# Kernel optimization log

Hardware: AMD Instinct MI355X
Metric: run time of the kernel (lower is better)

Reference implementation:

```python
import jax, jax.numpy as jnp
import numpy as np

NN_SIZE = 10  # matches init_kwargs nn_size


def _knn_idx(points, k):
    """points: (B,N,D). Returns (B,N,k) indices of k nearest neighbors, self excluded."""
    sq = jnp.sum(points * points, axis=-1)  # (B,N)
    # squared euclidean distances (B,N,N)
    d2 = sq[:, :, None] + sq[:, None, :] - 2.0 * jnp.einsum('bnd,bmd->bnm', points, points)
    _, idx = jax.lax.top_k(-d2, k + 1)  # smallest distances; first hit is self
    return idx[:, :, 1:]  # drop self -> (B,N,k)


def _uniform_laplacian(points, knn_idx):
    """points: (B,N,D); knn_idx: (B,N,K). lap = mean(neighbors) - point."""
    neigh = jax.vmap(lambda p, i: p[i])(points, knn_idx)  # (B,N,K,D) gather per batch
    return jnp.mean(neigh, axis=2) - points


def setup_inputs() -> dict:
    key = jax.random.key(0)
    k1, k2 = jax.random.split(key)
    B, N, D = 2, 8192, 3
    point1 = jax.random.normal(k1, (B, N, D), dtype=jnp.float32)
    point2 = jax.random.normal(k2, (B, N, D), dtype=jnp.float32)
    return {"point1": point1, "point2": point2}


def reference(point1, point2):
    knn_idx = _knn_idx(point1, NN_SIZE)          # connectivity from ref cloud
    lap1 = _uniform_laplacian(point1, knn_idx)   # (B,N,3)
    lap2 = _uniform_laplacian(point2, knn_idx)   # reuse knn_idx
    # metric = L1Loss (mean reduction); use_norm=False
    return jnp.mean(jnp.abs(lap1 - lap2))
```

## Files before the change

kernel.cpp:

```cpp
#include <hip/hip_runtime.h>
#include <math.h>


constexpr int NPTS  = 8192;
constexpr int NB    = 2;
constexpr int KNN   = 10;
constexpr int QPB   = 64;
constexpr int WPB   = 16;
constexpr int P1Q     = 32;
constexpr int P1BLOCK = P1Q * WPB;
constexpr int MVSTR   = WPB * KNN + 1;
constexpr int MASK13 = 0xFFFFE000;

constexpr int   G    = 32;
constexpr int   NC   = G * G * G;
constexpr float BMIN = -5.5f;
constexpr float BW   = 11.0f;
constexpr float H    = BW / G;
constexpr float INVH = (float)G / BW;

__device__ __forceinline__ void ins1(int l[KNN], int x) {
#pragma unroll
    for (int k = KNN - 1; k > 0; --k) l[k] = min(l[k], max(l[k - 1], x));
    l[0] = min(l[0], x);
}
__device__ __forceinline__ void ins2(int l[KNN], int a, int b) {
    const int b0 = min(a, b), b1 = max(a, b);
#pragma unroll
    for (int k = KNN - 1; k >= 2; --k)
        l[k] = min(l[k], min(max(l[k - 1], b0), max(l[k - 2], b1)));
    l[1] = min(l[1], min(max(l[0], b0), b1));
    l[0] = min(l[0], b0);
}
template<int S>
__device__ __forceinline__ void ins2s(int l[KNN], int a, int b) {
    const int b0 = min(a, b), b1 = max(a, b);
#pragma unroll
    for (int k = KNN - 1; k >= S + 2; --k)
        l[k] = min(l[k], min(max(l[k - 1], b0), max(l[k - 2], b1)));
    l[S + 1] = min(l[S + 1], min(max(l[S], b0), b1));
    l[S] = min(l[S], b0);
}
__device__ __forceinline__ void merge_sorted(int l[KNN], const int p[KNN]) {
    ins2s<0>(l, p[0], p[1]);
    ins2s<2>(l, p[2], p[3]);
    ins2s<4>(l, p[4], p[5]);
    ins2s<6>(l, p[6], p[7]);
    ins2s<8>(l, p[8], p[9]);
}

__global__ void pack_bin(const float* __restrict__ p1, float4* __restrict__ w,
                         int* __restrict__ hist, int* __restrict__ cellof,
                         float* __restrict__ out, int* __restrict__ nfail) {
    const int i = blockIdx.x * blockDim.x + threadIdx.x;
    if (i >= NB * NPTS) return;
    if (i == 0) { out[0] = 0.0f; nfail[0] = 0; }
    const float x = p1[3 * i], y = p1[3 * i + 1], z = p1[3 * i + 2];
    w[i] = make_float4(x, y, z, fmaf(x, x, fmaf(y, y, z * z)));
    const int cx = min(max((int)floorf((x - BMIN) * INVH), 0), G - 1);
    const int cy = min(max((int)floorf((y - BMIN) * INVH), 0), G - 1);
    const int cz = min(max((int)floorf((z - BMIN) * INVH), 0), G - 1);
    const int c = (cz << 10) | (cy << 5) | cx;
    cellof[i] = c;
    atomicAdd(&hist[(i >> 13) * NC + c], 1);
}

__global__ __launch_bounds__(1024)
void scan_cells(const int* __restrict__ hist, int* __restrict__ starts) {
    __shared__ int wsum[16];
    const int b = blockIdx.x, t = threadIdx.x;
    const int* hb = hist + b * NC;
    int* sb = starts + b * (NC + 1);
    const int c0 = t * 32;
    const int4* hb4 = (const int4*)(hb + c0);
    int loc[32]; int sum = 0;
#pragma unroll
    for (int j = 0; j < 8; ++j) {
        const int4 v = hb4[j];
        loc[4 * j + 0] = v.x; loc[4 * j + 1] = v.y;
        loc[4 * j + 2] = v.z; loc[4 * j + 3] = v.w;
        sum += v.x + v.y + v.z + v.w;
    }
    const int lane = t & 63, wvi = t >> 6;
    int incl = sum;
#pragma unroll
    for (int off = 1; off < 64; off <<= 1) {
        const int v = __shfl_up(incl, off);
        if (lane >= off) incl += v;
    }
    if (lane == 63) wsum[wvi] = incl;
    __syncthreads();
    if (t < 16) {
        const int v = wsum[t];
        int iv = v;
#pragma unroll
        for (int off = 1; off < 16; off <<= 1) {
            const int u = __shfl_up(iv, off);
            if (t >= off) iv += u;
        }
        wsum[t] = iv - v;
    }
    __syncthreads();
    int run = wsum[wvi] + incl - sum;
#pragma unroll
    for (int j = 0; j < 32; ++j) { sb[c0 + j] = run; run += loc[j]; }
    if (t == 1023) sb[NC] = run;
}

__global__ void scatter_all(const int* __restrict__ cellof,
                            const int* __restrict__ starts,
                            int* __restrict__ hist,
                            const float4* __restrict__ w,
                            const float* __restrict__ p2,
                            float4* __restrict__ wsorted,
                            float4* __restrict__ p2s) {
    const int i = blockIdx.x * blockDim.x + threadIdx.x;
    if (i >= NB * NPTS) return;
    const int b = i >> 13;
    const int c = cellof[i];
    const int old = atomicSub(&hist[b * NC + c], 1);
    const int pos = b * NPTS + starts[b * (NC + 1) + c] + old - 1;
    wsorted[pos] = w[i];
    p2s[pos] = make_float4(p2[3 * i], p2[3 * i + 1], p2[3 * i + 2], 0.0f);
}

template<int S>
__device__ __forceinline__ void scan_batched(const float4* __restrict__ W,
                                             const int* __restrict__ st,
                                             int cx, int cy, int cz,
                                             float m2x, float m2y, float m2z,
                                             float q2, int qpos, int sl,
                                             int l[KNN])
{
    constexpr int Wd = 2 * S + 1;
    constexpr int R  = Wd * Wd;
    constexpr int CH = 5;
    const int IMAX = 0x7FFFFFFF;
    int J0[R], J1[R];
#pragma unroll
    for (int r = 0; r < R; ++r) {
        const int dy = r % Wd - S, dz = r / Wd - S;
        const int ay = cy + dy, az = cz + dz;
        const bool ok = ((unsigned)ay < G) && ((unsigned)az < G);
        const int cbase = (az << 10) | (ay << 5);
        const int lo = cbase + max(cx - S, 0);
        const int hi = cbase + min(cx + S, G - 1) + 1;
        J0[r] = ok ? st[lo] : 0;
        J1[r] = ok ? st[hi] : 0;
    }
#pragma unroll
    for (int base = 0; base < R; base += CH) {
        float4 P[CH];
#pragma unroll
        for (int c = 0; c < CH; ++c) {
            const int r = base + c;
            if (r < R) {
                const int j = min(J0[r] + sl, NPTS - 1);
                P[c] = W[j];
            }
        }
#pragma unroll
        for (int c = 0; c < CH; ++c) {
            const int r = base + c;
            if (r < R) {
                const int j1 = J1[r];
                int j = J0[r] + sl;
                if (j < j1) {
                    float4 c4 = P[c];
                    while (true) {
                        const int jn = j + WPB;
                        const bool more = jn < j1;
                        float4 nx;
                        if (more) nx = W[jn];
                        const float d2 = fmaf(m2x, c4.x,
                                         fmaf(m2y, c4.y,
                                         fmaf(m2z, c4.z, c4.w + q2)));
                        int key = (__float_as_int(d2) & MASK13) | j;
                        key = (j == qpos) ? IMAX : key;
                        ins1(l, key);
                        if (!more) break;
                        c4 = nx; j = jn;
                    }
                }
            }
        }
    }
}

__global__ __launch_bounds__(P1BLOCK)
void phase1(const float4* __restrict__ wsorted, const float4* __restrict__ p2s,
            const int* __restrict__ starts, float* __restrict__ out,
            int* __restrict__ nfail, int* __restrict__ worklist)
{
    __shared__ int mv[P1Q * MVSTR];

    const int bid   = blockIdx.x;
    const int batch = bid & 1;
    const int g     = bid >> 1;
    const int tid   = threadIdx.x;
    const int qi    = tid >> 4;
    const int sl    = tid & 15;
    const int qpos  = (g << 5) + qi;

    const float4* W  = wsorted + batch * NPTS;
    const float4* P2 = p2s + batch * NPTS;
    const int*    st = starts + batch * (NC + 1);

    const float4 qp = W[qpos];
    const int cx = min(max((int)floorf((qp.x - BMIN) * INVH), 0), G - 1);
    const int cy = min(max((int)floorf((qp.y - BMIN) * INVH), 0), G - 1);
    const int cz = min(max((int)floorf((qp.z - BMIN) * INVH), 0), G - 1);
    const float lox = BMIN + cx * H, loy = BMIN + cy * H, loz = BMIN + cz * H;
    const float df = fminf(fminf(fminf(qp.x - lox, lox + H - qp.x),
                                 fminf(qp.y - loy, loy + H - qp.y)),
                           fminf(qp.z - loz, loz + H - qp.z));
    const float m2x = -2.0f * qp.x, m2y = -2.0f * qp.y, m2z = -2.0f * qp.z;
    const float q2 = qp.w;
    const int IMAX = 0x7FFFFFFF;

    const int sCov = (q2 > 4.8f) ? 2 : 1;

    int l[KNN];
#pragma unroll
    for (int k = 0; k < KNN; ++k) l[k] = IMAX;

    if (sCov == 1)
        scan_batched<1>(W, st, cx, cy, cz, m2x, m2y, m2z, q2, qpos, sl, l);
    else
        scan_batched<2>(W, st, cx, cy, cz, m2x, m2y, m2z, q2, qpos, sl, l);

#pragma unroll
    for (int k = 0; k < KNN; ++k) mv[qi * MVSTR + sl * KNN + k] = l[k];
    __syncthreads();

    float v = 0.0f;
    if (tid < P1Q) {
        int M[KNN];
#pragma unroll
        for (int k = 0; k < KNN; ++k) M[k] = IMAX;
#pragma unroll
        for (int e = 0; e < WPB; ++e) {
            int p[KNN];
#pragma unroll
            for (int k = 0; k < KNN; ++k) p[k] = mv[tid * MVSTR + e * KNN + k];
            merge_sorted(M, p);
        }

        const float tau = __int_as_float(M[KNN - 1] & MASK13);
        const float4 qq = W[(g << 5) + tid];
        const int sc = (qq.w > 4.8f) ? 2 : 1;
        const int qcx = min(max((int)floorf((qq.x - BMIN) * INVH), 0), G - 1);
        const int qcy = min(max((int)floorf((qq.y - BMIN) * INVH), 0), G - 1);
        const int qcz = min(max((int)floorf((qq.z - BMIN) * INVH), 0), G - 1);
        const float qlx = BMIN + qcx * H, qly = BMIN + qcy * H, qlz = BMIN + qcz * H;
        const float qdf = fminf(fminf(fminf(qq.x - qlx, qlx + H - qq.x),
                                      fminf(qq.y - qly, qly + H - qq.y)),
                                fminf(qq.z - qlz, qlz + H - qq.z));
        const float R = (float)sc * H + qdf;
        const bool covered = (tau <= R * R * 0.996f);
        if (covered) {
            float s1x = 0, s1y = 0, s1z = 0, s2x = 0, s2y = 0, s2z = 0;
#pragma unroll
            for (int k = 0; k < KNN; ++k) {
                const int j = M[k] & (NPTS - 1);
                const float4 c4 = W[j];
                const float4 n2 = P2[j];
                s1x += c4.x; s1y += c4.y; s1z += c4.z;
                s2x += n2.x; s2y += n2.y; s2z += n2.z;
            }
            const float4 p2v = P2[(g << 5) + tid];
            const float dx = (s1x * 0.1f - qq.x) - (s2x * 0.1f - p2v.x);
            const float dy2 = (s1y * 0.1f - qq.y) - (s2y * 0.1f - p2v.y);
            const float dz2 = (s1z * 0.1f - qq.z) - (s2z * 0.1f - p2v.z);
            v = fabsf(dx) + fabsf(dy2) + fabsf(dz2);
        } else {
            const int wi = atomicAdd(nfail, 1);
            worklist[wi] = (batch << 16) | ((g << 5) + tid);
        }
    }
    if (tid < 64) {
#pragma unroll
        for (int off = 32; off >= 1; off >>= 1) v += __shfl_down(v, off);
        if (tid == 0)
            atomicAdd(out, v * (1.0f / (float)(NB * NPTS * 3)));
    }
}

constexpr int P2BLK = 256;
constexpr int P2GRID = 512;

__global__ __launch_bounds__(P2BLK)
void phase2(const float4* __restrict__ wsorted, const float4* __restrict__ p2s,
            const int* __restrict__ nfail, const int* __restrict__ worklist,
            float* __restrict__ out)
{
    const int lane = threadIdx.x & 63;
    const int wv   = threadIdx.x >> 6;
    const int wid  = blockIdx.x * (P2BLK / 64) + wv;
    const int NW   = P2GRID * (P2BLK / 64);
    const int nf   = *nfail;
    const int IMAX = 0x7FFFFFFF;
    float acc = 0.0f;

    for (int i = wid; i < nf; i += NW) {
        const int e = worklist[i];
        const int batch = e >> 16, qpos = e & 0xFFFF;
        const float4* W  = wsorted + batch * NPTS;
        const float4* P2 = p2s + batch * NPTS;
        const float4 qp = W[qpos];
        const float m2x = -2.0f * qp.x, m2y = -2.0f * qp.y, m2z = -2.0f * qp.z;
        const float q2 = qp.w;

        int l[KNN];
#pragma unroll
        for (int k = 0; k < KNN; ++k) l[k] = IMAX;

#pragma unroll 2
        for (int it = 0; it < NPTS / 128; ++it) {
            const int ja = it * 128 + lane, jb = ja + 64;
            const float4 ca = W[ja];
            const float4 cb = W[jb];
            const float da = fmaf(m2x, ca.x, fmaf(m2y, ca.y, fmaf(m2z, ca.z, ca.w + q2)));
            const float db = fmaf(m2x, cb.x, fmaf(m2y, cb.y, fmaf(m2z, cb.z, cb.w + q2)));
            int ka = (__float_as_int(da) & MASK13) | ja;
            int kb = (__float_as_int(db) & MASK13) | jb;
            ka = (ja == qpos) ? IMAX : ka;
            kb = (jb == qpos) ? IMAX : kb;
            ins2(l, ka, kb);
        }
        for (int off = 1; off < 64; off <<= 1) {
            int p[KNN];
#pragma unroll
            for (int k = 0; k < KNN; ++k) p[k] = __shfl_xor(l[k], off);
            merge_sorted(l, p);
        }
        float s1x = 0, s1y = 0, s1z = 0, s2x = 0, s2y = 0, s2z = 0;
#pragma unroll
        for (int k = 0; k < KNN; ++k) {
            const int j = l[k] & (NPTS - 1);
            const float4 c4 = W[j];
            const float4 n2 = P2[j];
            s1x += c4.x; s1y += c4.y; s1z += c4.z;
            s2x += n2.x; s2y += n2.y; s2z += n2.z;
        }
        const float4 p2v = P2[qpos];
        const float dx = (s1x * 0.1f - qp.x) - (s2x * 0.1f - p2v.x);
        const float dy = (s1y * 0.1f - qp.y) - (s2y * 0.1f - p2v.y);
        const float dz = (s1z * 0.1f - qp.z) - (s2z * 0.1f - p2v.z);
        if (lane == 0) acc += fabsf(dx) + fabsf(dy) + fabsf(dz);
    }

    if (lane == 0 && acc != 0.0f)
        atomicAdd(out, acc * (1.0f / (float)(NB * NPTS * 3)));
}

constexpr int FB_WPB = 8;
constexpr int FB_BLOCK = QPB * FB_WPB;
constexpr int CHUNK = NPTS / FB_WPB;

__global__ void prep_pack(const float* __restrict__ p, float4* __restrict__ w) {
    const int i = blockIdx.x * blockDim.x + threadIdx.x;
    if (i < NB * NPTS) {
        const float x = p[3 * i], y = p[3 * i + 1], z = p[3 * i + 2];
        w[i] = make_float4(x, y, z, fmaf(x, x, fmaf(y, y, z * z)));
    }
}

__global__ __launch_bounds__(FB_BLOCK, 2)
void knn_lap(const float4* __restrict__ w1, const float* __restrict__ p2,
             float* __restrict__ out)
{
    __shared__ int mv[FB_WPB * KNN * QPB];
    const int batch = blockIdx.x >> 7;
    const int qbase = (blockIdx.x & 127) << 6;
    const int lane  = threadIdx.x & 63;
    const int wv    = __builtin_amdgcn_readfirstlane(threadIdx.x >> 6);
    const int query = qbase + lane;
    const float4* Wb = w1 + batch * NPTS;
    const float4 qp = Wb[query];
    const float m2x = -2.0f * qp.x, m2y = -2.0f * qp.y, m2z = -2.0f * qp.z;
    const float q2 = qp.w;
    const int IMAX = 0x7FFFFFFF;
    int l[KNN];
#pragma unroll
    for (int k = 0; k < KNN; ++k) l[k] = IMAX;
    const int c0 = wv * CHUNK;
    const float4* cand = Wb + c0;
#pragma unroll 4
    for (int i = 0; i < CHUNK; i += 2) {
        const float4 ca = cand[i];
        const float4 cb = cand[i + 1];
        const int ja = c0 + i, jb = ja + 1;
        const float da = fmaf(m2x, ca.x, fmaf(m2y, ca.y, fmaf(m2z, ca.z, ca.w + q2)));
        const float db = fmaf(m2x, cb.x, fmaf(m2y, cb.y, fmaf(m2z, cb.z, cb.w + q2)));
        int ka = (__float_as_int(da) & MASK13) | ja;
        int kb = (__float_as_int(db) & MASK13) | jb;
        ka = (ja == query) ? IMAX : ka;
        kb = (jb == query) ? IMAX : kb;
        ins2(l, ka, kb);
    }
#pragma unroll
    for (int k = 0; k < KNN; ++k) mv[(wv * KNN + k) * QPB + lane] = l[k];
    __syncthreads();
    if (threadIdx.x < QPB) {
        int m[KNN];
#pragma unroll
        for (int k = 0; k < KNN; ++k) m[k] = IMAX;
#pragma unroll
        for (int e = 0; e < FB_WPB; ++e) {
            int p[KNN];
#pragma unroll
            for (int k = 0; k < KNN; ++k) p[k] = mv[(e * KNN + k) * QPB + lane];
            merge_sorted(m, p);
        }
        const float* P2b = p2 + (size_t)batch * NPTS * 3;
        float s1x = 0, s1y = 0, s1z = 0, s2x = 0, s2y = 0, s2z = 0;
#pragma unroll
        for (int k = 0; k < KNN; ++k) {
            const int j = m[k] & (NPTS - 1);
            const float4 c = Wb[j];
            s1x += c.x; s1y += c.y; s1z += c.z;
            s2x += P2b[3 * j + 0]; s2y += P2b[3 * j + 1]; s2z += P2b[3 * j + 2];
        }
        const int q = qbase + threadIdx.x;
        const float p2x = P2b[3 * q + 0], p2y = P2b[3 * q + 1], p2z = P2b[3 * q + 2];
        const float dx = (s1x * 0.1f - qp.x) - (s2x * 0.1f - p2x);
        const float dy = (s1y * 0.1f - qp.y) - (s2y * 0.1f - p2y);
        const float dz = (s1z * 0.1f - qp.z) - (s2z * 0.1f - p2z);
        float v = fabsf(dx) + fabsf(dy) + fabsf(dz);
#pragma unroll
        for (int off = 32; off >= 1; off >>= 1) v += __shfl_down(v, off);
        if (threadIdx.x == 0)
            atomicAdd(out, v * (1.0f / (float)(NB * NPTS * 3)));
    }
}

extern "C" void kernel_launch(void* const* d_in, const int* in_sizes, int n_in,
                              void* d_out, int out_size, void* d_ws, size_t ws_size,
                              hipStream_t stream) {
    const float* p1 = (const float*)d_in[0];
    const float* p2 = (const float*)d_in[1];
    float* out = (float*)d_out;

    size_t off = 0;
    float4* w       = (float4*)d_ws;               off += (size_t)NB * NPTS * 16;
    int*    hist    = (int*)((char*)d_ws + off);   off += (size_t)NB * NC * 4;
    int*    starts  = (int*)((char*)d_ws + off);   off += (size_t)NB * (NC + 1) * 4 + 8;
    int*    cellof  = (int*)((char*)d_ws + off);   off += (size_t)NB * NPTS * 4;
    float4* wsorted = (float4*)((char*)d_ws + off); off += (size_t)NB * NPTS * 16;
    float4* p2s     = (float4*)((char*)d_ws + off); off += (size_t)NB * NPTS * 16;
    int*    nfail   = (int*)((char*)d_ws + off);   off += 16;
    int*    worklist= (int*)((char*)d_ws + off);   off += (size_t)NB * NPTS * 4;

    if (ws_size < off) {
        hipMemsetAsync(out, 0, sizeof(float), stream);
        prep_pack<<<(NB * NPTS + 255) / 256, 256, 0, stream>>>(p1, w);
        knn_lap<<<NB * (NPTS / QPB), FB_BLOCK, 0, stream>>>(w, p2, out);
        return;
    }

    hipMemsetAsync(hist, 0, (size_t)NB * NC * 4, stream);
    pack_bin<<<(NB * NPTS + 255) / 256, 256, 0, stream>>>(p1, w, hist, cellof,
                                                          out, nfail);
    scan_cells<<<NB, 1024, 0, stream>>>(hist, starts);
    scatter_all<<<(NB * NPTS + 255) / 256, 256, 0, stream>>>(cellof, starts, hist,
                                                             w, p2, wsorted, p2s);
    phase1<<<NB * (NPTS / P1Q), P1BLOCK, 0, stream>>>(wsorted, p2s, starts, out,
                                                      nfail, worklist);
    phase2<<<P2GRID, P2BLK, 0, stream>>>(wsorted, p2s, nfail, worklist, out);
}
```

Before: 116.5 us.

## Fuse binning, scan and scatter into one shared-memory counting-sort kernel

Replaces the memset plus three kernels (pack_bin, scan_cells, scatter_all) with a single build_all kernel that runs one 1024-thread block per batch. That block builds the cell histogram with shared-memory atomics on an XOR-swizzled index, scans it in place and scatters both point clouds. This removes three launches, the global histogram atomics and the intermediate w/cellof buffers. The cost is only two blocks of parallelism and a 128KB shared-memory footprint, so the sort runs serially on two CUs.

```diff
diff --git a/kernel.cpp b/kernel.cpp
--- a/kernel.cpp
+++ b/kernel.cpp
@@ -19,6 +19,8 @@
 constexpr float H    = BW / G;
 constexpr float INVH = (float)G / BW;
 
+__device__ __forceinline__ int SW(int c) { return c ^ ((c >> 5) & 31); }
+
 __device__ __forceinline__ void ins1(int l[KNN], int x) {
 #pragma unroll
     for (int k = KNN - 1; k > 0; --k) l[k] = min(l[k], max(l[k - 1], x));
@@ -49,79 +51,91 @@
     ins2s<8>(l, p[8], p[9]);
 }
 
-__global__ void pack_bin(const float* __restrict__ p1, float4* __restrict__ w,
-                         int* __restrict__ hist, int* __restrict__ cellof,
-                         float* __restrict__ out, int* __restrict__ nfail) {
-    const int i = blockIdx.x * blockDim.x + threadIdx.x;
-    if (i >= NB * NPTS) return;
-    if (i == 0) { out[0] = 0.0f; nfail[0] = 0; }
-    const float x = p1[3 * i], y = p1[3 * i + 1], z = p1[3 * i + 2];
-    w[i] = make_float4(x, y, z, fmaf(x, x, fmaf(y, y, z * z)));
-    const int cx = min(max((int)floorf((x - BMIN) * INVH), 0), G - 1);
-    const int cy = min(max((int)floorf((y - BMIN) * INVH), 0), G - 1);
-    const int cz = min(max((int)floorf((z - BMIN) * INVH), 0), G - 1);
-    const int c = (cz << 10) | (cy << 5) | cx;
-    cellof[i] = c;
-    atomicAdd(&hist[(i >> 13) * NC + c], 1);
-}
-
-__global__ __launch_bounds__(1024)
-void scan_cells(const int* __restrict__ hist, int* __restrict__ starts) {
-    __shared__ int wsum[16];
-    const int b = blockIdx.x, t = threadIdx.x;
-    const int* hb = hist + b * NC;
+constexpr int BB = 1024;
+constexpr int PPT = NPTS / BB;
+
+__global__ __launch_bounds__(BB)
+void build_all(const float* __restrict__ p1, const float* __restrict__ p2,
+               int* __restrict__ starts, float4* __restrict__ wsorted,
+               float4* __restrict__ p2s, float* __restrict__ out,
+               int* __restrict__ nfail)
+{
+    __shared__ unsigned int hcur[NC];
+    __shared__ int wsum[BB / 64];
+
+    const int b = blockIdx.x;
+    const int t = threadIdx.x;
+    if (b == 0 && t == 0) { out[0] = 0.0f; nfail[0] = 0; }
+
+#pragma unroll
+    for (int j = 0; j < NC / BB; ++j) hcur[t + BB * j] = 0u;
+    __syncthreads();
+
+    const float* P1 = p1 + (size_t)b * NPTS * 3;
+    float4 r[6];
+    {
+        const float4* P14 = (const float4*)P1;
+#pragma unroll
+        for (int j = 0; j < 6; ++j) r[j] = P14[t * 6 + j];
+    }
+    const float* rf = (const float*)r;
+    float px[PPT], py[PPT], pz[PPT], pw[PPT]; int pc[PPT];
+#pragma unroll
+    for (int j = 0; j < PPT; ++j) {
+        const float x = rf[3 * j], y = rf[3 * j + 1], z = rf[3 * j + 2];
+        px[j] = x; py[j] = y; pz[j] = z;
+        pw[j] = fmaf(x, x, fmaf(y, y, z * z));
+        const int cx = min(max((int)floorf((x - BMIN) * INVH), 0), G - 1);
+        const int cy = min(max((int)floorf((y - BMIN) * INVH), 0), G - 1);
+        const int cz = min(max((int)floorf((z - BMIN) * INVH), 0), G - 1);
+        pc[j] = (cz << 10) | (cy << 5) | cx;
+        atomicAdd(&hcur[SW(pc[j])], 1u);
+    }
+    __syncthreads();
+
+    const int c0 = t * 32;
+    unsigned int sum = 0;
+#pragma unroll
+    for (int j = 0; j < 32; ++j) sum += hcur[SW(c0 + j)];
+    const int lane = t & 63, wvi = t >> 6;
+    unsigned int incl = sum;
+#pragma unroll
+    for (int off = 1; off < 64; off <<= 1) {
+        const unsigned int u = __shfl_up(incl, off);
+        if (lane >= off) incl += u;
+    }
+    if (lane == 63) wsum[wvi] = (int)incl;
+    __syncthreads();
+    unsigned int woff = 0;
+    for (int e = 0; e < wvi; ++e) woff += (unsigned int)wsum[e];
+    unsigned int run = woff + incl - sum;
     int* sb = starts + b * (NC + 1);
-    const int c0 = t * 32;
-    const int4* hb4 = (const int4*)(hb + c0);
-    int loc[32]; int sum = 0;
-#pragma unroll
-    for (int j = 0; j < 8; ++j) {
-        const int4 v = hb4[j];
-        loc[4 * j + 0] = v.x; loc[4 * j + 1] = v.y;
-        loc[4 * j + 2] = v.z; loc[4 * j + 3] = v.w;
-        sum += v.x + v.y + v.z + v.w;
-    }
-    const int lane = t & 63, wvi = t >> 6;
-    int incl = sum;
-#pragma unroll
-    for (int off = 1; off < 64; off <<= 1) {
-        const int v = __shfl_up(incl, off);
-        if (lane >= off) incl += v;
-    }
-    if (lane == 63) wsum[wvi] = incl;
-    __syncthreads();
-    if (t < 16) {
-        const int v = wsum[t];
-        int iv = v;
-#pragma unroll
-        for (int off = 1; off < 16; off <<= 1) {
-            const int u = __shfl_up(iv, off);
-            if (t >= off) iv += u;
-        }
-        wsum[t] = iv - v;
-    }
-    __syncthreads();
-    int run = wsum[wvi] + incl - sum;
-#pragma unroll
-    for (int j = 0; j < 32; ++j) { sb[c0 + j] = run; run += loc[j]; }
-    if (t == 1023) sb[NC] = run;
-}
-
-__global__ void scatter_all(const int* __restrict__ cellof,
-                            const int* __restrict__ starts,
-                            int* __restrict__ hist,
-                            const float4* __restrict__ w,
-                            const float* __restrict__ p2,
-                            float4* __restrict__ wsorted,
-                            float4* __restrict__ p2s) {
-    const int i = blockIdx.x * blockDim.x + threadIdx.x;
-    if (i >= NB * NPTS) return;
-    const int b = i >> 13;
-    const int c = cellof[i];
-    const int old = atomicSub(&hist[b * NC + c], 1);
-    const int pos = b * NPTS + starts[b * (NC + 1) + c] + old - 1;
-    wsorted[pos] = w[i];
-    p2s[pos] = make_float4(p2[3 * i], p2[3 * i + 1], p2[3 * i + 2], 0.0f);
+#pragma unroll
+    for (int j = 0; j < 32; ++j) {
+        const unsigned int cnt = hcur[SW(c0 + j)];
+        sb[c0 + j] = (int)run;
+        hcur[SW(c0 + j)] = run;
+        run += cnt;
+    }
+    if (t == BB - 1) sb[NC] = (int)run;
+    __syncthreads();
+
+    const float* P2 = p2 + (size_t)b * NPTS * 3;
+    float4 r2[6];
+    {
+        const float4* P24 = (const float4*)P2;
+#pragma unroll
+        for (int j = 0; j < 6; ++j) r2[j] = P24[t * 6 + j];
+    }
+    const float* rf2 = (const float*)r2;
+    const int base = b * NPTS;
+#pragma unroll
+    for (int j = 0; j < PPT; ++j) {
+        const unsigned int pos = atomicAdd(&hcur[SW(pc[j])], 1u);
+        const int gp = base + (int)pos;
+        wsorted[gp] = make_float4(px[j], py[j], pz[j], pw[j]);
+        p2s[gp] = make_float4(rf2[3 * j], rf2[3 * j + 1], rf2[3 * j + 2], 0.0f);
+    }
 }
 
 template<int S>
@@ -449,8 +463,9 @@
     int*    cellof  = (int*)((char*)d_ws + off);   off += (size_t)NB * NPTS * 4;
     float4* wsorted = (float4*)((char*)d_ws + off); off += (size_t)NB * NPTS * 16;
     float4* p2s     = (float4*)((char*)d_ws + off); off += (size_t)NB * NPTS * 16;
-    int*    nfail   = (int*)((char*)d_ws + off);   off += 16;
+    int*    nfail   = (int*)((char*)d_ws + off);   off += 512;
     int*    worklist= (int*)((char*)d_ws + off);   off += (size_t)NB * NPTS * 4;
+    (void)hist; (void)cellof;
 
     if (ws_size < off) {
         hipMemsetAsync(out, 0, sizeof(float), stream);
@@ -459,12 +474,7 @@
         return;
     }
 
-    hipMemsetAsync(hist, 0, (size_t)NB * NC * 4, stream);
-    pack_bin<<<(NB * NPTS + 255) / 256, 256, 0, stream>>>(p1, w, hist, cellof,
-                                                          out, nfail);
-    scan_cells<<<NB, 1024, 0, stream>>>(hist, starts);
-    scatter_all<<<(NB * NPTS + 255) / 256, 256, 0, stream>>>(cellof, starts, hist,
-                                                             w, p2, wsorted, p2s);
+    build_all<<<NB, BB, 0, stream>>>(p1, p2, starts, wsorted, p2s, out, nfail);
     phase1<<<NB * (NPTS / P1Q), P1BLOCK, 0, stream>>>(wsorted, p2s, starts, out,
                                                       nfail, worklist);
     phase2<<<P2GRID, P2BLK, 0, stream>>>(wsorted, p2s, nfail, worklist, out);
```

New measurement: 118.2 us. Within noise of the previous version (+1.4%).
